# Performance work log

Hardware: AMD Instinct MI355X
Metric: run time of the kernel (lower is better)

## Reference

```python
import jax, jax.numpy as jnp
import numpy as np

N, E, IN, H, OUT, G = 50000, 800000, 128, 256, 10, 512


def setup_inputs() -> dict:
    key = jax.random.key(0)
    ks = jax.random.split(key, 12)
    def lin(k, fan_in, fan_out):
        s = 1.0 / np.sqrt(fan_in)
        kw, kb = jax.random.split(k)
        W = jax.random.uniform(kw, (fan_in, fan_out), jnp.float32, -s, s)
        b = jax.random.uniform(kb, (fan_out,), jnp.float32, -s, s)
        return W, b
    x = jax.random.normal(ks[0], (N, IN), jnp.float32)
    edge_index = jax.random.randint(ks[1], (2, E), 0, N)
    batch = jnp.sort(jax.random.randint(ks[2], (N,), 0, G))
    W1a, b1a = lin(ks[3], IN, H)
    W1b, b1b = lin(ks[4], H, H)
    W2a, b2a = lin(ks[5], H, H)
    W2b, b2b = lin(ks[6], H, H)
    Wlin, blin = lin(ks[7], H, OUT)
    eps1 = jnp.zeros((), jnp.float32)
    eps2 = jnp.zeros((), jnp.float32)
    return dict(x=x, edge_index=edge_index, batch=batch,
                eps1=eps1, W1a=W1a, b1a=b1a, W1b=W1b, b1b=b1b,
                eps2=eps2, W2a=W2a, b2a=b2a, W2b=W2b, b2b=b2b,
                Wlin=Wlin, blin=blin)


def reference(x, edge_index, batch, eps1, W1a, b1a, W1b, b1b,
              eps2, W2a, b2a, W2b, b2b, Wlin, blin):
    src, dst = edge_index[0], edge_index[1]
    # GINConv 1: h = MLP((1+eps)*x + sum_{j in N(i)} x_j)
    agg = jax.ops.segment_sum(x[src], dst, num_segments=N)  # [N, IN]
    h = (1.0 + eps1) * x + agg
    h = jax.nn.relu(h @ W1a + b1a) @ W1b + b1b              # [N, H]
    h = jax.nn.relu(h)  # (dropout p=0.3 is identity in eval mode)
    # GINConv 2
    agg2 = jax.ops.segment_sum(h[src], dst, num_segments=N)  # [N, H]
    h2 = (1.0 + eps2) * h + agg2
    h2 = jax.nn.relu(h2 @ W2a + b2a) @ W2b + b2b             # [N, H]
    # global mean pool per graph
    psum = jax.ops.segment_sum(h2, batch, num_segments=G)    # [G, H]
    cnt = jax.ops.segment_sum(jnp.ones((N, 1), h2.dtype), batch, num_segments=G)
    pooled = psum / jnp.maximum(cnt, 1.0)
    out = pooled @ Wlin + blin                               # [G, OUT]
    return jax.nn.log_softmax(out, axis=-1)
```

## Files before the change

kernel.cpp:

```cpp
#include <hip/hip_runtime.h>
#include <math.h>
#include <stdint.h>

constexpr int N   = 50000;
constexpr int E   = 800000;
constexpr int IN  = 128;
constexpr int H   = 256;
constexpr int OUT = 10;
constexpr int G   = 512;
constexpr int BSTR = 64;

constexpr int NPART  = 391;
constexpr int SEGCAP = 48;
constexpr int EPB    = 4096;
constexpr int AB     = (E + EPB - 1) / EPB;

typedef __bf16 bf16x8 __attribute__((ext_vector_type(8)));
typedef float  f32x4  __attribute__((ext_vector_type(4)));
typedef float  f32x2  __attribute__((ext_vector_type(2)));

__device__ __forceinline__ float blo(unsigned v) { return __uint_as_float(v << 16); }
__device__ __forceinline__ float bhi(unsigned v) { return __uint_as_float(v & 0xffff0000u); }
__device__ __forceinline__ unsigned short f2b(float f) {
  unsigned u = __float_as_uint(f);
  u += 0x7fffu + ((u >> 16) & 1u);
  return (unsigned short)(u >> 16);
}
__device__ __forceinline__ unsigned packb(float lo, float hi) {
  return (unsigned)f2b(lo) | ((unsigned)f2b(hi) << 16);
}
__device__ __forceinline__ unsigned pk_fp8x4(float a, float b, float c, float d) {
  int r = 0;
  r = __builtin_amdgcn_cvt_pk_fp8_f32(a, b, r, false);
  r = __builtin_amdgcn_cvt_pk_fp8_f32(c, d, r, true);
  return (unsigned)r;
}
__device__ __forceinline__ unsigned char fp8_1(float v) {
  return (unsigned char)(__builtin_amdgcn_cvt_pk_fp8_f32(v, v, 0, false) & 0xff);
}

__device__ __forceinline__ void acc8(float* a, uint2 w, float s) {
  unsigned ws[2] = {w.x, w.y};
#pragma unroll
  for (int d = 0; d < 2; ++d) {
    f32x2 lo = __builtin_amdgcn_cvt_pk_f32_fp8((int)ws[d], false);
    f32x2 hi = __builtin_amdgcn_cvt_pk_f32_fp8((int)ws[d], true);
    a[4*d+0] = fmaf(s, lo.x, a[4*d+0]);
    a[4*d+1] = fmaf(s, lo.y, a[4*d+1]);
    a[4*d+2] = fmaf(s, hi.x, a[4*d+2]);
    a[4*d+3] = fmaf(s, hi.y, a[4*d+3]);
  }
}


constexpr int XQ_BLOCKS  = (N * IN / 4) / 256;
constexpr int W1A_BLOCKS = (256 * IN) / 256;
constexpr int WH_BLOCKS  = (256 * H) / 256;

__global__ __launch_bounds__(256) void prep_kernel(
    const int* __restrict__ srcp, const int* __restrict__ dstp,
    unsigned* __restrict__ pbuf, int* __restrict__ pcnt,
    const float* __restrict__ x, unsigned* __restrict__ xq,
    const float* __restrict__ W1a, unsigned short* __restrict__ Wt1a,
    const float* __restrict__ W1b, unsigned short* __restrict__ Wt1b,
    const float* __restrict__ W2a, unsigned short* __restrict__ Wt2a,
    const float* __restrict__ W2b, unsigned short* __restrict__ Wt2b) {
  __shared__ int lcur[NPART];
  int b = blockIdx.x;
  int t = threadIdx.x;
  if (b < AB) {
    for (int j = t; j < NPART; j += 256) lcur[j] = 0;
    __syncthreads();
    const int e0 = b * EPB;
#pragma unroll
    for (int r = 0; r < EPB / 1024; ++r) {
      int base = e0 + (r * 256 + t) * 4;
      if (base < E) {
        int4 d4 = *(const int4*)(dstp + base);
        int4 s4 = *(const int4*)(srcp + base);
        int dd[4] = {d4.x, d4.y, d4.z, d4.w};
        int ss[4] = {s4.x, s4.y, s4.z, s4.w};
#pragma unroll
        for (int u = 0; u < 4; ++u) {
          int part = dd[u] >> 7, dl = dd[u] & 127;
          int pos = atomicAdd(&lcur[part], 1);
          if (pos < SEGCAP)
            pbuf[((size_t)part * AB + b) * SEGCAP + pos] =
                ((unsigned)dl << 16) | (unsigned)ss[u];
        }
      }
    }
    __syncthreads();
    for (int j = t; j < NPART; j += 256) pcnt[b * NPART + j] = min(lcur[j], SEGCAP);
    return;
  }
  b -= AB;
  if (b < XQ_BLOCKS) {
    int id = b * 256 + t;
    float4 v = ((const float4*)x)[id];
    xq[id] = pk_fp8x4(v.x, v.y, v.z, v.w);
    return;
  }
  b -= XQ_BLOCKS;
  if (b < W1A_BLOCKS) {
    int id = b * 256 + t;
    int n = id >> 7, k = id & 127;
    Wt1a[id] = f2b(W1a[k * 256 + n]);
    return;
  }
  b -= W1A_BLOCKS;
  const float* Ws;
  unsigned short* Wd;
  if (b < WH_BLOCKS)            { Ws = W1b; Wd = Wt1b; }
  else if (b < 2 * WH_BLOCKS)   { Ws = W2a; Wd = Wt2a; b -= WH_BLOCKS; }
  else                          { Ws = W2b; Wd = Wt2b; b -= 2 * WH_BLOCKS; }
  int id = b * 256 + t;
  int n = id >> 8, k = id & 255;
  Wd[id] = f2b(Ws[k * 256 + n]);
}


__global__ __launch_bounds__(256) void csr_kernel(const unsigned* __restrict__ pbuf,
                                                  const int* __restrict__ pcnt,
                                                  int* __restrict__ deg, int* __restrict__ csre) {
  __shared__ int sa[256], sb[256];
  __shared__ int ldeg[128];
  int p = blockIdx.x;
  int t = threadIdx.x;
  if (t < 128) ldeg[t] = 0;
  sa[t] = (t < AB) ? pcnt[t * NPART + p] : 0;
  __syncthreads();
  int* cur = sa; int* nxt = sb;
#pragma unroll
  for (int off = 1; off < 256; off <<= 1) {
    nxt[t] = cur[t] + ((t >= off) ? cur[t - off] : 0);
    __syncthreads();
    int* tmp = cur; cur = nxt; nxt = tmp;
  }
  int T = cur[255];
  const unsigned* seg = pbuf + (size_t)p * AB * SEGCAP;
  for (int f = t; f < T; f += 256) {
    int lo = 0, hi = AB - 1;
    while (lo < hi) { int m = (lo + hi) >> 1; if (cur[m] > f) hi = m; else lo = m + 1; }
    int bb = lo;
    int excl = bb ? cur[bb - 1] : 0;
    unsigned v = seg[(size_t)bb * SEGCAP + (f - excl)];
    int dl = (int)(v >> 16), s = (int)(v & 0xFFFFu);
    int pos = atomicAdd(&ldeg[dl], 1);
    if (pos < BSTR) csre[(((size_t)p << 7) + dl) * BSTR + pos] = s;
  }
  __syncthreads();
  if (t < 128) {
    int node = (p << 7) + t;
    if (node < N) deg[node] = min(ldeg[t], BSTR);
  }
}


template <int K1, bool RELU2, bool OUT8>
__global__ __launch_bounds__(256, 3) void fused_mlp_kernel(
    const unsigned char* __restrict__ inq,
    const int* __restrict__ deg, const int* __restrict__ csre,
    const float* __restrict__ epsp,
    const unsigned short* __restrict__ Bta,
    const float* __restrict__ ba,
    const unsigned short* __restrict__ Btb,
    const float* __restrict__ bb,
    void* __restrict__ outv, int Nrows) {
  constexpr int LDK = 40;
  constexpr int LDA = K1 + 40;
  constexpr int LDI = H + 40;
  constexpr int KSL = K1 / 64;
  __shared__ __align__(16) unsigned short sh[10240 + 32 * LDI];
  unsigned short* Bs = sh;
  unsigned short* Af = sh + 10240;
  unsigned short* Is = sh + 10240;
  const int tid  = threadIdx.x;
  const int r0   = blockIdx.x * 32;
  const int wave = tid >> 6, lane = tid & 63;
  const int quad = lane >> 4, l15 = lane & 15;
  const int wcol = wave * 64;
  const int srow = tid >> 2;
  const int sk8  = (tid & 3) * 8;

  {
    const float sc = 1.0f + epsp[0];
    const int slot = tid & 7;
    const int nd0  = tid >> 3;
    const int i = r0 + nd0;
    const int* bkt = csre + (size_t)i * BSTR;
    int dg = 0;
    if (i < Nrows) { dg = deg[i]; if (dg > BSTR) dg = BSTR; }
    for (int ps = 0; ps < KSL; ++ps) {
      const unsigned char* rb = inq + ps * 64 + slot * 8;
      float a[8];
#pragma unroll
      for (int q = 0; q < 8; ++q) a[q] = 0.f;
      int j = 0;
      for (; j + 8 <= dg; j += 8) {
        unsigned idx[8];
#pragma unroll
        for (int u = 0; u < 8; ++u) {
          unsigned raw = (unsigned)bkt[j + u];
          idx[u] = raw < (unsigned)N ? raw : 0u;
        }
        uint2 v[8];
#pragma unroll
        for (int u = 0; u < 8; ++u)
          v[u] = *(const uint2*)(rb + (size_t)idx[u] * K1);
#pragma unroll
        for (int u = 0; u < 8; ++u) acc8(a, v[u], 1.0f);
      }
      for (; j < dg; ++j) {
        unsigned raw = (unsigned)bkt[j];
        if (raw >= (unsigned)N) raw = 0u;
        acc8(a, *(const uint2*)(rb + (size_t)raw * K1), 1.0f);
      }
      if (i < Nrows)
        acc8(a, *(const uint2*)(rb + (size_t)i * K1), sc);
      *(uint4*)(Af + nd0 * LDA + ps * 64 + slot * 8) =
          make_uint4(packb(a[0], a[1]), packb(a[2], a[3]),
                     packb(a[4], a[5]), packb(a[6], a[7]));
    }
  }

  f32x4 acc1[2][4];
#pragma unroll
  for (int i = 0; i < 2; ++i)
#pragma unroll
    for (int j = 0; j < 4; ++j) acc1[i][j] = (f32x4){0.f, 0.f, 0.f, 0.f};

  for (int k0 = 0; k0 < K1; k0 += 32) {
#pragma unroll
    for (int sgm = 0; sgm < 4; ++sgm) {
      int col = srow + sgm * 64;
      *(uint4*)(Bs + col * LDK + sk8) = *(const uint4*)(Bta + (size_t)col * K1 + k0 + sk8);
    }
    __syncthreads();
    bf16x8 af[2];
#pragma unroll
    for (int mt = 0; mt < 2; ++mt)
      af[mt] = *(const bf16x8*)(Af + (mt * 16 + l15) * LDA + k0 + quad * 8);
    bf16x8 bfr[4];
#pragma unroll
    for (int nt = 0; nt < 4; ++nt)
      bfr[nt] = *(const bf16x8*)(Bs + (wcol + nt * 16 + l15) * LDK + quad * 8);
#pragma unroll
    for (int mt = 0; mt < 2; ++mt)
#pragma unroll
      for (int nt = 0; nt < 4; ++nt)
        acc1[mt][nt] =
            __builtin_amdgcn_mfma_f32_16x16x32_bf16(af[mt], bfr[nt], acc1[mt][nt], 0, 0, 0);
    __syncthreads();
  }

  float bva[4];
#pragma unroll
  for (int nt = 0; nt < 4; ++nt) bva[nt] = ba[wcol + nt * 16 + l15];

#pragma unroll
  for (int mt = 0; mt < 2; ++mt)
#pragma unroll
    for (int nt = 0; nt < 4; ++nt) {
      int col = wcol + nt * 16 + l15;
      int rbase = mt * 16 + quad * 4;
#pragma unroll
      for (int i = 0; i < 4; ++i)
        Is[(rbase + i) * LDI + col] = f2b(fmaxf(acc1[mt][nt][i] + bva[nt], 0.f));
    }
  __syncthreads();

  f32x4 acc2[2][4];
#pragma unroll
  for (int i = 0; i < 2; ++i)
#pragma unroll
    for (int j = 0; j < 4; ++j) acc2[i][j] = (f32x4){0.f, 0.f, 0.f, 0.f};

  for (int kk = 0; kk < H / 32; ++kk) {
    const int k0 = kk * 32;
#pragma unroll
    for (int sgm = 0; sgm < 4; ++sgm) {
      int col = srow + sgm * 64;
      *(uint4*)(Bs + col * LDK + sk8) = *(const uint4*)(Btb + (size_t)col * 256 + k0 + sk8);
    }
    __syncthreads();
    bf16x8 af[2];
#pragma unroll
    for (int mt = 0; mt < 2; ++mt)
      af[mt] = *(const bf16x8*)(Is + (mt * 16 + l15) * LDI + k0 + quad * 8);
    bf16x8 bfr[4];
#pragma unroll
    for (int nt = 0; nt < 4; ++nt)
      bfr[nt] = *(const bf16x8*)(Bs + (wcol + nt * 16 + l15) * LDK + quad * 8);
#pragma unroll
    for (int mt = 0; mt < 2; ++mt)
#pragma unroll
      for (int nt = 0; nt < 4; ++nt)
        acc2[mt][nt] =
            __builtin_amdgcn_mfma_f32_16x16x32_bf16(af[mt], bfr[nt], acc2[mt][nt], 0, 0, 0);
    __syncthreads();
  }

  float bv[4];
#pragma unroll
  for (int nt = 0; nt < 4; ++nt) bv[nt] = bb[wcol + nt * 16 + l15];
#pragma unroll
  for (int mt = 0; mt < 2; ++mt) {
    int gr0 = r0 + mt * 16 + quad * 4;
#pragma unroll
    for (int i = 0; i < 4; ++i) {
      int grow = gr0 + i;
      if (grow >= Nrows) continue;
#pragma unroll
      for (int nt = 0; nt < 4; ++nt) {
        float v = acc2[mt][nt][i] + bv[nt];
        if (RELU2) v = fmaxf(v, 0.f);
        int col = wcol + nt * 16 + l15;
        if (OUT8) ((unsigned char*)outv)[(size_t)grow * 256 + col] = fp8_1(v);
        else      ((unsigned short*)outv)[(size_t)grow * 256 + col] = f2b(v);
      }
    }
  }
}


__global__ __launch_bounds__(128) void pool_final_kernel(const unsigned short* __restrict__ h2,
                                                         const int* __restrict__ batch,
                                                         const float* __restrict__ Wlin,
                                                         const float* __restrict__ blin,
                                                         float* __restrict__ out) {
  __shared__ float sp[H];
  __shared__ float logits[OUT];
  int g = blockIdx.x;
  int t = threadIdx.x;
  int lo = 0, hi = N;
  while (lo < hi) { int m = (lo + hi) >> 1; if (batch[m] < g) lo = m + 1; else hi = m; }
  int s = lo;
  lo = 0; hi = N;
  while (lo < hi) { int m = (lo + hi) >> 1; if (batch[m] < g + 1) lo = m + 1; else hi = m; }
  int e = lo;
  float a0 = 0.f, a1 = 0.f;
  const unsigned* base = (const unsigned*)h2;
  int n = s;
  for (; n + 4 <= e; n += 4) {
    unsigned v0 = base[(size_t)(n + 0) * (H / 2) + t];
    unsigned v1 = base[(size_t)(n + 1) * (H / 2) + t];
    unsigned v2 = base[(size_t)(n + 2) * (H / 2) + t];
    unsigned v3 = base[(size_t)(n + 3) * (H / 2) + t];
    a0 += blo(v0) + blo(v1) + blo(v2) + blo(v3);
    a1 += bhi(v0) + bhi(v1) + bhi(v2) + bhi(v3);
  }
  for (; n < e; ++n) {
    unsigned v = base[(size_t)n * (H / 2) + t];
    a0 += blo(v); a1 += bhi(v);
  }
  float inv = 1.0f / fmaxf((float)(e - s), 1.0f);
  sp[2 * t]     = a0 * inv;
  sp[2 * t + 1] = a1 * inv;
  __syncthreads();
  if (t < OUT) {
    float acc = blin[t];
    for (int k = 0; k < H; ++k) acc = fmaf(sp[k], Wlin[k * OUT + t], acc);
    logits[t] = acc;
  }
  __syncthreads();
  if (t == 0) {
    float m = -INFINITY;
    for (int j = 0; j < OUT; ++j) m = fmaxf(m, logits[j]);
    float ssum = 0.f;
    for (int j = 0; j < OUT; ++j) ssum += expf(logits[j] - m);
    float ls = logf(ssum);
    for (int j = 0; j < OUT; ++j) out[(size_t)g * OUT + j] = logits[j] - m - ls;
  }
}


static inline char* align_up(char* p, size_t a) {
  return (char*)(((uintptr_t)p + a - 1) & ~(a - 1));
}

extern "C" void kernel_launch(void* const* d_in, const int* in_sizes, int n_in,
                              void* d_out, int out_size, void* d_ws, size_t ws_size,
                              hipStream_t stream) {
  const float* x    = (const float*)d_in[0];
  const int*   ei   = (const int*)d_in[1];
  const int*   srcp = ei;
  const int*   dstp = ei + E;
  const int*   batch = (const int*)d_in[2];
  const float* eps1 = (const float*)d_in[3];
  const float* W1a  = (const float*)d_in[4];
  const float* b1a  = (const float*)d_in[5];
  const float* W1b  = (const float*)d_in[6];
  const float* b1b  = (const float*)d_in[7];
  const float* eps2 = (const float*)d_in[8];
  const float* W2a  = (const float*)d_in[9];
  const float* b2a  = (const float*)d_in[10];
  const float* W2b  = (const float*)d_in[11];
  const float* b2b  = (const float*)d_in[12];
  const float* Wlin = (const float*)d_in[13];
  const float* blin = (const float*)d_in[14];
  float* outp = (float*)d_out;

  char* p = (char*)d_ws;
  unsigned* pbuf = (unsigned*)p;     p = align_up(p + (size_t)NPART * AB * SEGCAP * 4, 256);
  int* pcnt = (int*)p;               p = align_up(p + (size_t)AB * NPART * 4, 256);
  int* deg  = (int*)p;               p = align_up(p + (size_t)N * 4, 256);
  int* csre = (int*)p;               p = align_up(p + (size_t)NPART * 128 * BSTR * 4, 256);
  unsigned* xq = (unsigned*)p;       p = align_up(p + (size_t)N * IN, 256);
  unsigned char* h1q = (unsigned char*)p;  p = align_up(p + (size_t)N * H, 256);
  unsigned short* B2 = (unsigned short*)p; p = align_up(p + (size_t)N * H * 2, 256);
  unsigned short* Wt1a = (unsigned short*)p;  p = align_up(p + (size_t)H * IN * 2, 256);
  unsigned short* Wt1b = (unsigned short*)p;  p = align_up(p + (size_t)H * H * 2, 256);
  unsigned short* Wt2a = (unsigned short*)p;  p = align_up(p + (size_t)H * H * 2, 256);
  unsigned short* Wt2b = (unsigned short*)p;  p = align_up(p + (size_t)H * H * 2, 256);

  prep_kernel<<<AB + XQ_BLOCKS + W1A_BLOCKS + 3 * WH_BLOCKS, 256, 0, stream>>>(
      srcp, dstp, pbuf, pcnt, x, xq, W1a, Wt1a, W1b, Wt1b, W2a, Wt2a, W2b, Wt2b);

  csr_kernel<<<NPART, 256, 0, stream>>>(pbuf, pcnt, deg, csre);

  const int nb = (N + 31) / 32;

  fused_mlp_kernel<IN, true, true><<<nb, 256, 0, stream>>>(
      (const unsigned char*)xq, deg, csre, eps1, Wt1a, b1a, Wt1b, b1b, h1q, N);

  fused_mlp_kernel<H, false, false><<<nb, 256, 0, stream>>>(
      h1q, deg, csre, eps2, Wt2a, b2a, Wt2b, b2b, B2, N);

  pool_final_kernel<<<G, 128, 0, stream>>>(B2, batch, Wlin, blin, outp);
}
```

Before: 283.1 us.

## Split gather-aggregation into XCD-sliced kernel ahead of the MLP GEMMs

Takes the neighbor gather/sum out of the fused MLP kernel and moves it into a separate kernel. That kernel assigns each 64-column feature slice to a fixed group of XCDs by block-index interleaving, so each XCD's L2 only caches its own slice of the gathered source rows. The bf16 aggregate is written to a new global buffer, and the MLP kernel now just loads tiles from it. The cost is an extra launch per layer and an extra round trip of the aggregate through memory (N×K1 bf16 written and then read back). It also relies on the assumption that blocks are dispatched round-robin across the 8 XCDs.

```diff
diff --git a/kernel.cpp b/kernel.cpp
--- a/kernel.cpp
+++ b/kernel.cpp
@@ -14,6 +14,8 @@
 constexpr int SEGCAP = 48;
 constexpr int EPB    = 4096;
 constexpr int AB     = (E + EPB - 1) / EPB;
+constexpr int NB32   = (N + 31) / 32;
+constexpr int NPAD   = NB32 * 32;
 
 typedef __bf16 bf16x8 __attribute__((ext_vector_type(8)));
 typedef float  f32x4  __attribute__((ext_vector_type(4)));
@@ -157,11 +159,62 @@
 }
 
 
-template <int K1, bool RELU2, bool OUT8>
-__global__ __launch_bounds__(256, 3) void fused_mlp_kernel(
+template <int K1>
+__global__ __launch_bounds__(256) void agg_slice_kernel(
     const unsigned char* __restrict__ inq,
     const int* __restrict__ deg, const int* __restrict__ csre,
     const float* __restrict__ epsp,
+    unsigned short* __restrict__ agg) {
+  constexpr int KSL = K1 / 64;
+  constexpr int XPS = 8 / KSL;
+  const int vb  = blockIdx.x;
+  const int xcd = vb & 7;
+  const int q   = vb >> 3;
+  const int slice = xcd / XPS;
+  const int tile  = q * XPS + (xcd & (XPS - 1));
+  if (tile >= NB32) return;
+  const int tid  = threadIdx.x;
+  const int slot = tid & 7;
+  const int nd0  = tid >> 3;
+  const int i = tile * 32 + nd0;
+  if (i >= N) return;
+  const float sc = 1.0f + epsp[0];
+  const unsigned char* rb = inq + slice * 64 + slot * 8;
+  const int* bkt = csre + (size_t)i * BSTR;
+  int dg = deg[i]; if (dg > BSTR) dg = BSTR;
+  float a[8];
+#pragma unroll
+  for (int qf = 0; qf < 8; ++qf) a[qf] = 0.f;
+  int j = 0;
+  for (; j + 8 <= dg; j += 8) {
+    unsigned idx[8];
+#pragma unroll
+    for (int u = 0; u < 8; ++u) {
+      unsigned raw = (unsigned)bkt[j + u];
+      idx[u] = raw < (unsigned)N ? raw : 0u;
+    }
+    uint2 v[8];
+#pragma unroll
+    for (int u = 0; u < 8; ++u)
+      v[u] = *(const uint2*)(rb + (size_t)idx[u] * K1);
+#pragma unroll
+    for (int u = 0; u < 8; ++u) acc8(a, v[u], 1.0f);
+  }
+  for (; j < dg; ++j) {
+    unsigned raw = (unsigned)bkt[j];
+    if (raw >= (unsigned)N) raw = 0u;
+    acc8(a, *(const uint2*)(rb + (size_t)raw * K1), 1.0f);
+  }
+  acc8(a, *(const uint2*)(rb + (size_t)i * K1), sc);
+  *(uint4*)(agg + (size_t)i * K1 + slice * 64 + slot * 8) =
+      make_uint4(packb(a[0], a[1]), packb(a[2], a[3]),
+                 packb(a[4], a[5]), packb(a[6], a[7]));
+}
+
+
+template <int K1, bool RELU2, bool OUT8>
+__global__ __launch_bounds__(256, 3) void mlp_kernel(
+    const unsigned short* __restrict__ A,
     const unsigned short* __restrict__ Bta,
     const float* __restrict__ ba,
     const unsigned short* __restrict__ Btb,
@@ -170,7 +223,6 @@
   constexpr int LDK = 40;
   constexpr int LDA = K1 + 40;
   constexpr int LDI = H + 40;
-  constexpr int KSL = K1 / 64;
   __shared__ __align__(16) unsigned short sh[10240 + 32 * LDI];
   unsigned short* Bs = sh;
   unsigned short* Af = sh + 10240;
@@ -183,45 +235,12 @@
   const int srow = tid >> 2;
   const int sk8  = (tid & 3) * 8;
 
-  {
-    const float sc = 1.0f + epsp[0];
-    const int slot = tid & 7;
-    const int nd0  = tid >> 3;
-    const int i = r0 + nd0;
-    const int* bkt = csre + (size_t)i * BSTR;
-    int dg = 0;
-    if (i < Nrows) { dg = deg[i]; if (dg > BSTR) dg = BSTR; }
-    for (int ps = 0; ps < KSL; ++ps) {
-      const unsigned char* rb = inq + ps * 64 + slot * 8;
-      float a[8];
-#pragma unroll
-      for (int q = 0; q < 8; ++q) a[q] = 0.f;
-      int j = 0;
-      for (; j + 8 <= dg; j += 8) {
-        unsigned idx[8];
-#pragma unroll
-        for (int u = 0; u < 8; ++u) {
-          unsigned raw = (unsigned)bkt[j + u];
-          idx[u] = raw < (unsigned)N ? raw : 0u;
-        }
-        uint2 v[8];
-#pragma unroll
-        for (int u = 0; u < 8; ++u)
-          v[u] = *(const uint2*)(rb + (size_t)idx[u] * K1);
-#pragma unroll
-        for (int u = 0; u < 8; ++u) acc8(a, v[u], 1.0f);
-      }
-      for (; j < dg; ++j) {
-        unsigned raw = (unsigned)bkt[j];
-        if (raw >= (unsigned)N) raw = 0u;
-        acc8(a, *(const uint2*)(rb + (size_t)raw * K1), 1.0f);
-      }
-      if (i < Nrows)
-        acc8(a, *(const uint2*)(rb + (size_t)i * K1), sc);
-      *(uint4*)(Af + nd0 * LDA + ps * 64 + slot * 8) =
-          make_uint4(packb(a[0], a[1]), packb(a[2], a[3]),
-                     packb(a[4], a[5]), packb(a[6], a[7]));
-    }
+#pragma unroll
+  for (int u = 0; u < K1 / 64; ++u) {
+    int id  = u * 256 + tid;
+    int row = id / (K1 / 8);
+    int kk  = (id % (K1 / 8)) * 8;
+    *(uint4*)(Af + row * LDA + kk) = *(const uint4*)(A + (size_t)(r0 + row) * K1 + kk);
   }
 
   f32x4 acc1[2][4];
@@ -409,6 +428,8 @@
   unsigned* xq = (unsigned*)p;       p = align_up(p + (size_t)N * IN, 256);
   unsigned char* h1q = (unsigned char*)p;  p = align_up(p + (size_t)N * H, 256);
   unsigned short* B2 = (unsigned short*)p; p = align_up(p + (size_t)N * H * 2, 256);
+  unsigned short* Agg1 = (unsigned short*)p; p = align_up(p + (size_t)NPAD * IN * 2, 256);
+  unsigned short* Agg2 = (unsigned short*)p; p = align_up(p + (size_t)NPAD * H * 2, 256);
   unsigned short* Wt1a = (unsigned short*)p;  p = align_up(p + (size_t)H * IN * 2, 256);
   unsigned short* Wt1b = (unsigned short*)p;  p = align_up(p + (size_t)H * H * 2, 256);
   unsigned short* Wt2a = (unsigned short*)p;  p = align_up(p + (size_t)H * H * 2, 256);
@@ -419,13 +440,15 @@
 
   csr_kernel<<<NPART, 256, 0, stream>>>(pbuf, pcnt, deg, csre);
 
-  const int nb = (N + 31) / 32;
-
-  fused_mlp_kernel<IN, true, true><<<nb, 256, 0, stream>>>(
-      (const unsigned char*)xq, deg, csre, eps1, Wt1a, b1a, Wt1b, b1b, h1q, N);
-
-  fused_mlp_kernel<H, false, false><<<nb, 256, 0, stream>>>(
-      h1q, deg, csre, eps2, Wt2a, b2a, Wt2b, b2b, B2, N);
+  agg_slice_kernel<IN><<<8 * ((NB32 + 3) / 4), 256, 0, stream>>>(
+      (const unsigned char*)xq, deg, csre, eps1, Agg1);
+  mlp_kernel<IN, true, true><<<NB32, 256, 0, stream>>>(
+      Agg1, Wt1a, b1a, Wt1b, b1b, h1q, N);
+
+  agg_slice_kernel<H><<<8 * ((NB32 + 1) / 2), 256, 0, stream>>>(
+      h1q, deg, csre, eps2, Agg2);
+  mlp_kernel<H, false, false><<<NB32, 256, 0, stream>>>(
+      Agg2, Wt2a, b2a, Wt2b, b2b, B2, N);
 
   pool_final_kernel<<<G, 128, 0, stream>>>(B2, batch, Wlin, blin, outp);
 }
```

Result: no change. 280.2 us (-1.0%).
